# Kernel tuning notes

Measured on AMD Instinct MI355X. Metric: run time of the kernel, lower is better.

The kernel has to match this reference:

```python
import jax, jax.numpy as jnp
import numpy as np

B, H, W, P, DEPTH = 128, 512, 512, 64, 4
EPS = 1e-5


def _std(t):
    # torch.std default: unbiased (ddof=1), over last two dims, keepdim
    m = t.mean(axis=(-2, -1), keepdims=True)
    n = t.shape[-1] * t.shape[-2]
    var = ((t - m) ** 2).sum(axis=(-2, -1), keepdims=True) / (n - 1)
    return jnp.sqrt(var)


def _flat_softmax(t):
    # softmax over all non-batch dims (flatten(1).softmax(1).reshape)
    b = t.shape[0]
    return jax.nn.softmax(t.reshape(b, -1), axis=1).reshape(t.shape)


def setup_inputs() -> dict:
    key = jax.random.key(0)
    ks = jax.random.split(key, 9)
    # xavier-uniform-like scale for [*, fan_in, fan_out] params
    def init(k, shape):
        fan_in, fan_out = shape[-2], shape[-1]
        gain = float(np.sqrt(2.0))  # relu gain
        bound = gain * float(np.sqrt(6.0 / (fan_in + fan_out)))
        return jax.random.uniform(k, shape, jnp.float32, -bound, bound)
    return {
        "x": jax.random.normal(ks[0], (B, H, W), jnp.float32),
        "o_xj": init(ks[1], (DEPTH, W, P)),
        "o_xi": init(ks[2], (DEPTH, H, P)),
        "p_xj": init(ks[3], (DEPTH, H, P)),
        "p_xi": init(ks[4], (DEPTH, W, P)),
        "o_rel_xj": init(ks[5], (DEPTH, W, P)),
        "o_rel_xi": init(ks[6], (DEPTH, H, P)),
        "p_rel_xj": init(ks[7], (DEPTH, P, P)),
        "p_rel_xi": init(ks[8], (DEPTH, P, P)),
    }


def reference(x, o_xj, o_xi, p_xj, p_xi, o_rel_xj, o_rel_xi, p_rel_xj, p_rel_xi):
    # eval-mode forward (dropout inactive)
    b, h, w = x.shape
    p = o_xj.shape[-1]
    depth = o_xj.shape[0]
    scale = (h / p) * (w / p)
    x_mean = x.mean(axis=(-2, -1), keepdims=True) * scale  # [B,1,1]
    x_std = _std(x) * scale                                 # [B,1,1]
    xt = jnp.swapaxes(x, -1, -2)                            # [B,W,H]

    projection = jnp.zeros((b, p, p), jnp.float32)
    for d in range(depth):
        # relevance branches on original orientation
        o_rel_xj_sum = _flat_softmax(x @ o_rel_xj[d]).sum(axis=-2)   # [B,P]
        o_rel_xi_sum = _flat_softmax(xt @ o_rel_xi[d]).sum(axis=-2)  # [B,P]
        # projection branches
        o_t_xj = x @ o_xj[d]                                # [B,H,P]
        o_t_xi = xt @ o_xi[d]                               # [B,W,P]
        p_t_xj = jnp.swapaxes(o_t_xj, -1, -2) @ p_xj[d]     # [B,P,P]
        p_t_xi = jnp.swapaxes(o_t_xi, -1, -2) @ p_xi[d]     # [B,P,P]
        # relevance branches on permuted projection
        p_rel_xj_sum = _flat_softmax(p_t_xj @ p_rel_xj[d]).sum(axis=-2)  # [B,P]
        p_rel_xi_sum = _flat_softmax(p_t_xi @ p_rel_xi[d]).sum(axis=-2)  # [B,P]
        f_j = jnp.sqrt(o_rel_xj_sum / p_rel_xj_sum)         # [B,P]
        f_i = jnp.sqrt(o_rel_xi_sum / p_rel_xi_sum)         # [B,P]
        x_buf = p_t_xj * f_j[..., None] + jnp.swapaxes(p_t_xi * f_i[..., None], -1, -2)
        # renormalize to original (scaled) statistics
        x_buf = (x_buf - x_buf.mean(axis=(-2, -1), keepdims=True)) / (_std(x_buf) + EPS)
        x_buf = x_buf * x_std + x_mean
        projection = projection + x_buf
    return projection
```

## Files before the change

kernel.cpp:

```cpp
#include <hip/hip_runtime.h>
#include <math.h>

typedef __attribute__((ext_vector_type(8))) short short8;
typedef __attribute__((ext_vector_type(4))) short short4v;
typedef __attribute__((ext_vector_type(4))) float f32x4;

#define EPSF 1e-5f

__device__ __forceinline__ short f2bf(float f) {
    union { float f; unsigned u; } v; v.f = f;
    unsigned r = (v.u + 0x7FFFu + ((v.u >> 16) & 1u)) >> 16;
    return (short)r;
}

__device__ __forceinline__ void gload16(const void* g, void* l) {
    __builtin_amdgcn_global_load_lds(
        (const __attribute__((address_space(1))) unsigned int*)g,
        (__attribute__((address_space(3))) unsigned int*)l, 16, 0, 0);
}

__global__ __launch_bounds__(256) void xprep_kernel(const float* __restrict__ x,
                                                    short* __restrict__ xbf,
                                                    short* __restrict__ xtbf,
                                                    double* __restrict__ part) {
    int blk = blockIdx.x;
    int b = blk >> 6, t = blk & 63;
    int tr = (t >> 3) * 64, tc = (t & 7) * 64;
    const float* X = x + (size_t)b * 262144;
    __shared__ short tileR[64][80];
    __shared__ double rs[256], rq[256];
    int tid = threadIdx.x;

    {
        int r = tid >> 2, cseg = (tid & 3) * 16;
        const float* src = X + (size_t)(tr + r) * 512 + tc + cseg;
        double s = 0.0, sq = 0.0;
        short vals[16];
        #pragma unroll
        for (int q = 0; q < 4; q++) {
            float4 f = *(const float4*)(src + q * 4);
            vals[q * 4 + 0] = f2bf(f.x); vals[q * 4 + 1] = f2bf(f.y);
            vals[q * 4 + 2] = f2bf(f.z); vals[q * 4 + 3] = f2bf(f.w);
            s += (double)f.x + (double)f.y + (double)f.z + (double)f.w;
            sq += (double)f.x * f.x + (double)f.y * f.y + (double)f.z * f.z + (double)f.w * f.w;
        }
        *(short8*)&tileR[r][cseg]     = *(short8*)&vals[0];
        *(short8*)&tileR[r][cseg + 8] = *(short8*)&vals[8];
        rs[tid] = s; rq[tid] = sq;
    }
    __syncthreads();
    for (int st = 128; st > 0; st >>= 1) {
        if (tid < st) { rs[tid] += rs[tid + st]; rq[tid] += rq[tid + st]; }
        __syncthreads();
    }
    if (tid == 0) { part[blk * 2] = rs[0]; part[blk * 2 + 1] = rq[0]; }

    int w = tid >> 6, l = tid & 63, li = l & 15, lg = l >> 4;
    #pragma unroll
    for (int q = 0; q < 2; q++) {
        int cc = w * 2 + q;
        int Rl = cc >> 1, ktl = cc & 1;
        short8 v = *(const short8*)&tileR[Rl * 16 + li][ktl * 32 + lg * 8];
        size_t chunk = (size_t)(b * 32 + (tr >> 4) + Rl) * 16 + (tc >> 5) + ktl;
        *(short8*)(xbf + chunk * 512 + l * 8) = v;
    }
    #pragma unroll
    for (int q = 0; q < 2; q++) {
        int cc = w * 2 + q;
        int Rl = cc >> 1, ktl = cc & 1;
        int c_loc = Rl * 16 + li;
        int rbase = ktl * 32 + lg * 8;
        short8 v;
        #pragma unroll
        for (int e = 0; e < 8; e++) v[e] = tileR[rbase + e][c_loc];
        size_t chunk = (size_t)(b * 32 + (tc >> 4) + Rl) * 16 + (tr >> 5) + ktl;
        *(short8*)(xtbf + chunk * 512 + l * 8) = v;
    }
}

__global__ __launch_bounds__(256) void stats_p1(const float* __restrict__ x,
                                                double* __restrict__ part) {
    int blk = blockIdx.x;
    const float4* X = (const float4*)(x + (size_t)blk * 65536);
    double s = 0.0, sq = 0.0;
    for (int i = threadIdx.x; i < 16384; i += 256) {
        float4 v = X[i];
        s += (double)v.x + (double)v.y + (double)v.z + (double)v.w;
        sq += (double)v.x * v.x + (double)v.y * v.y + (double)v.z * v.z + (double)v.w * v.w;
    }
    __shared__ double rs[256], rq[256];
    rs[threadIdx.x] = s; rq[threadIdx.x] = sq;
    __syncthreads();
    for (int st = 128; st > 0; st >>= 1) {
        if (threadIdx.x < st) { rs[threadIdx.x] += rs[threadIdx.x + st]; rq[threadIdx.x] += rq[threadIdx.x + st]; }
        __syncthreads();
    }
    if (threadIdx.x == 0) { part[blk * 2] = rs[0]; part[blk * 2 + 1] = rq[0]; }
}

__global__ void stats_p2(const double* __restrict__ part, float* __restrict__ stats, int ppb) {
    int b = threadIdx.x;
    double s = 0.0, sq = 0.0;
    for (int p = 0; p < ppb; p++) { s += part[(b * ppb + p) * 2]; sq += part[(b * ppb + p) * 2 + 1]; }
    double n = 262144.0;
    double mean = s / n;
    double var = (sq - n * mean * mean) / (n - 1.0);
    stats[b * 2 + 0] = (float)(mean * 64.0);
    stats[b * 2 + 1] = (float)(sqrt(var) * 64.0);
}

__global__ __launch_bounds__(256) void wprep_kernel(
    const float* __restrict__ o_xj, const float* __restrict__ o_xi,
    const float* __restrict__ p_xj, const float* __restrict__ p_xi,
    const float* __restrict__ o_rel_xj, const float* __restrict__ o_rel_xi,
    short* __restrict__ wcat, short* __restrict__ wpt) {
    int idx = blockIdx.x * 256 + threadIdx.x;
    if (idx < 65536) {
        int l = idx & 63; int chunk = idx >> 6;
        int kt = chunk & 15, ns = (chunk >> 4) & 7, sd = chunk >> 7;
        int side = sd >> 2, dd = sd & 3;
        int n = ns * 16 + (l & 15);
        int k = kt * 32 + (l >> 4) * 8;
        const float* src = (n < 64) ? (side ? o_rel_xi : o_rel_xj)
                                    : (side ? o_xi : o_xj);
        src += (size_t)dd * 32768 + (n & 63);
        short8 v;
        #pragma unroll
        for (int e = 0; e < 8; e++) v[e] = f2bf(src[(size_t)(k + e) * 64]);
        *(short8*)(wcat + (size_t)chunk * 512 + l * 8) = v;
    } else {
        int j = idx - 65536;
        int l = j & 63; int chunk = j >> 6;
        int nq = chunk & 3, kk = (chunk >> 2) & 3, mt = (chunk >> 4) & 3, sd = chunk >> 6;
        int side = sd >> 2, dd = sd & 3;
        int q = nq * 16 + (l & 15);
        int r = mt * 128 + kk * 32 + (l >> 4) * 8;
        const float* src = (side ? p_xi : p_xj) + (size_t)dd * 32768 + q;
        short8 v;
        #pragma unroll
        for (int e = 0; e < 8; e++) v[e] = f2bf(src[(size_t)(r + e) * 64]);
        *(short8*)(wpt + (size_t)chunk * 512 + l * 8) = v;
    }
}

__global__ __launch_bounds__(256, 3) void main_mfma_kernel(
    const short* __restrict__ xbf, const short* __restrict__ xtbf,
    const short* __restrict__ wcat, const short* __restrict__ wpt,
    float* __restrict__ relsum, float* __restrict__ pt) {
    int blk = blockIdx.x;
    int xcd = blk & 7, rest = blk >> 3;
    int d = rest & 3, side = (rest >> 2) & 1, bhi = rest >> 3;
    int b = bhi * 8 + xcd;
    const short* Xsw = (side ? xtbf : xbf) + (size_t)b * 262144;
    const short* Wc  = wcat + (size_t)(side * 4 + d) * 65536;
    const short* Wp  = wpt + (size_t)(side * 4 + d) * 32768;

    __shared__ __align__(16) char lds[33792];
    short* Xs  = (short*)lds;
    short* Wsh = (short*)(lds + 8192);
    short* Tos = (short*)lds;
    short* Wps = (short*)(lds + 17408);

    int tid = threadIdx.x;
    int w = tid >> 6, l = tid & 63, li = l & 15, lg = l >> 4;
    int wm = w >> 1, wn = w & 1;

    f32x4 zero4 = {0.f, 0.f, 0.f, 0.f};
    f32x4 ptacc[4];
    #pragma unroll
    for (int i = 0; i < 4; i++) ptacc[i] = zero4;
    float esum[4] = {0.f, 0.f, 0.f, 0.f};

    for (int mt = 0; mt < 4; mt++) {
        f32x4 acc[4][4];
        #pragma unroll
        for (int i = 0; i < 4; i++)
            #pragma unroll
            for (int j = 0; j < 4; j++) acc[i][j] = zero4;

        for (int kt = 0; kt < 16; kt++) {
            __syncthreads();
            #pragma unroll
            for (int ii = 0; ii < 4; ii++) {
                int s = w * 4 + ii;
                if (s < 8)
                    gload16(Xsw + ((size_t)((mt * 8 + s) * 16 + kt)) * 512 + l * 8, Xs + s * 512);
                else
                    gload16(Wc + ((size_t)((s - 8) * 16 + kt)) * 512 + l * 8, Wsh + (s - 8) * 512);
            }
            __syncthreads();
            short8 af[4], bfv[4];
            #pragma unroll
            for (int i = 0; i < 4; i++) af[i] = *(const short8*)(Xs + (wm * 4 + i) * 512 + l * 8);
            #pragma unroll
            for (int j = 0; j < 4; j++) bfv[j] = *(const short8*)(Wsh + (wn * 4 + j) * 512 + l * 8);
            #pragma unroll
            for (int i = 0; i < 4; i++)
                #pragma unroll
                for (int j = 0; j < 4; j++)
                    acc[i][j] = __builtin_amdgcn_mfma_f32_16x16x32_bf16(af[i], bfv[j], acc[i][j], 0, 0, 0);
        }

        #pragma unroll
        for (int ii = 0; ii < 4; ii++) {
            int s = w * 4 + ii;
            gload16(Wp + ((size_t)((mt * 4 + (s >> 2)) * 4 + (s & 3))) * 512 + l * 8, Wps + s * 512);
        }
        __syncthreads();

        if (wn == 0) {
            #pragma unroll
            for (int i = 0; i < 4; i++)
                #pragma unroll
                for (int j = 0; j < 4; j++)
                    esum[j] += __expf(acc[i][j][0]) + __expf(acc[i][j][1]) +
                               __expf(acc[i][j][2]) + __expf(acc[i][j][3]);
        } else {
            #pragma unroll
            for (int i = 0; i < 4; i++)
                #pragma unroll
                for (int j = 0; j < 4; j++) {
                    int p = j * 16 + li;
                    int rb = wm * 64 + i * 16 + lg * 4;
                    short4v tv;
                    tv.x = f2bf(acc[i][j][0]); tv.y = f2bf(acc[i][j][1]);
                    tv.z = f2bf(acc[i][j][2]); tv.w = f2bf(acc[i][j][3]);
                    *(short4v*)(Tos + p * 136 + rb) = tv;
                }
        }
        __syncthreads();

        #pragma unroll
        for (int kk = 0; kk < 4; kk++) {
            short8 a = *(const short8*)(Tos + (w * 16 + li) * 136 + kk * 32 + lg * 8);
            #pragma unroll
            for (int nq = 0; nq < 4; nq++) {
                short8 bb = *(const short8*)(Wps + (kk * 4 + nq) * 512 + l * 8);
                ptacc[nq] = __builtin_amdgcn_mfma_f32_16x16x32_bf16(a, bb, ptacc[nq], 0, 0, 0);
            }
        }
    }

    __syncthreads();
    float* red = (float*)lds;
    if (wn == 0) {
        #pragma unroll
        for (int j = 0; j < 4; j++) red[wm * 256 + l * 4 + j] = esum[j];
    }
    __syncthreads();
    size_t base = (size_t)(b * 2 + side) * 4 + d;
    if (tid < 64) {
        float s = 0.f;
        #pragma unroll
        for (int w2 = 0; w2 < 2; w2++)
            #pragma unroll
            for (int g = 0; g < 4; g++)
                s += red[w2 * 256 + (g * 16 + (tid & 15)) * 4 + (tid >> 4)];
        float tot = s;
        #pragma unroll
        for (int off = 1; off < 64; off <<= 1) tot += __shfl_xor(tot, off, 64);
        relsum[base * 64 + tid] = s / tot;
    }
    float* ptout = pt + base * 4096;
    #pragma unroll
    for (int nq = 0; nq < 4; nq++)
        #pragma unroll
        for (int r = 0; r < 4; r++)
            ptout[(size_t)(w * 16 + lg * 4 + r) * 64 + nq * 16 + li] = ptacc[nq][r];
}

__global__ __launch_bounds__(256) void fused_proj_kernel(
    const float* __restrict__ x,
    const float* __restrict__ o_xj, const float* __restrict__ o_xi,
    const float* __restrict__ p_xj, const float* __restrict__ p_xi,
    const float* __restrict__ o_rel_xj, const float* __restrict__ o_rel_xi,
    float* __restrict__ relsum, float* __restrict__ pt)
{
    int blk = blockIdx.x;
    int b = blk >> 3;
    int side = (blk >> 2) & 1;
    int d = blk & 3;

    const float* Wrel = (side ? o_rel_xi : o_rel_xj) + (size_t)d * (512 * 64);
    const float* Wo   = (side ? o_xi     : o_xj)     + (size_t)d * (512 * 64);
    const float* Wp   = (side ? p_xi     : p_xj)     + (size_t)d * (512 * 64);
    const float* X = x + (size_t)b * (512 * 512);

    __shared__ float Xs[16][68];
    __shared__ float Ws[16][128];
    __shared__ float To[64][68];
    __shared__ float Wps[64][68];
    __shared__ float red[16][64];
    __shared__ float cs[64];
    __shared__ float total_s;

    int tid = threadIdx.x;
    int tx = tid & 15;
    int ty = tid >> 4;

    float paccum[4][4];
    #pragma unroll
    for (int i = 0; i < 4; i++)
        #pragma unroll
        for (int j = 0; j < 4; j++) paccum[i][j] = 0.f;
    float esum[8];
    #pragma unroll
    for (int j = 0; j < 8; j++) esum[j] = 0.f;

    for (int r0 = 0; r0 < 512; r0 += 64) {
        float acc[4][8];
        #pragma unroll
        for (int i = 0; i < 4; i++)
            #pragma unroll
            for (int j = 0; j < 8; j++) acc[i][j] = 0.f;

        for (int k0 = 0; k0 < 512; k0 += 16) {
            if (side == 0) {
                int kk = tid & 15, r = tid >> 4;
                #pragma unroll
                for (int it = 0; it < 4; it++, r += 16)
                    Xs[kk][r] = X[(size_t)(r0 + r) * 512 + (k0 + kk)];
            } else {
                int r = tid & 63, kk = tid >> 6;
                #pragma unroll
                for (int it = 0; it < 4; it++, kk += 4)
                    Xs[kk][r] = X[(size_t)(k0 + kk) * 512 + (r0 + r)];
            }
            {
                int c = tid & 127, kk = tid >> 7;
                const float* Wsrc = (c < 64) ? (Wrel + c) : (Wo + (c - 64));
                #pragma unroll
                for (int it = 0; it < 8; it++, kk += 2)
                    Ws[kk][c] = Wsrc[(size_t)(k0 + kk) * 64];
            }
            __syncthreads();
            #pragma unroll
            for (int kk = 0; kk < 16; kk++) {
                float4 a  = *(const float4*)&Xs[kk][ty * 4];
                float4 b0 = *(const float4*)&Ws[kk][tx * 8];
                float4 b1 = *(const float4*)&Ws[kk][tx * 8 + 4];
                float av[4] = {a.x, a.y, a.z, a.w};
                float bv[8] = {b0.x, b0.y, b0.z, b0.w, b1.x, b1.y, b1.z, b1.w};
                #pragma unroll
                for (int i = 0; i < 4; i++)
                    #pragma unroll
                    for (int j = 0; j < 8; j++)
                        acc[i][j] = fmaf(av[i], bv[j], acc[i][j]);
            }
            __syncthreads();
        }

        if (tx < 8) {
            #pragma unroll
            for (int i = 0; i < 4; i++)
                #pragma unroll
                for (int j = 0; j < 8; j++)
                    esum[j] += expf(acc[i][j]);
        } else {
            #pragma unroll
            for (int i = 0; i < 4; i++) {
                float4 v0 = make_float4(acc[i][0], acc[i][1], acc[i][2], acc[i][3]);
                float4 v1 = make_float4(acc[i][4], acc[i][5], acc[i][6], acc[i][7]);
                *(float4*)&To[ty * 4 + i][(tx - 8) * 8]     = v0;
                *(float4*)&To[ty * 4 + i][(tx - 8) * 8 + 4] = v1;
            }
        }
        {
            int q = tid & 63, r = tid >> 6;
            #pragma unroll
            for (int it = 0; it < 16; it++, r += 4)
                Wps[r][q] = Wp[(size_t)(r0 + r) * 64 + q];
        }
        __syncthreads();
        for (int r = 0; r < 64; r++) {
            float4 aa = *(const float4*)&To[r][ty * 4];
            float4 bb = *(const float4*)&Wps[r][tx * 4];
            float av[4] = {aa.x, aa.y, aa.z, aa.w};
            float bv[4] = {bb.x, bb.y, bb.z, bb.w};
            #pragma unroll
            for (int i = 0; i < 4; i++)
                #pragma unroll
                for (int j = 0; j < 4; j++)
                    paccum[i][j] = fmaf(av[i], bv[j], paccum[i][j]);
        }
        __syncthreads();
    }

    if (tx < 8) {
        #pragma unroll
        for (int j = 0; j < 8; j++) red[ty][tx * 8 + j] = esum[j];
    }
    __syncthreads();
    if (tid < 64) {
        float s = 0.f;
        for (int t = 0; t < 16; t++) s += red[t][tid];
        cs[tid] = s;
    }
    __syncthreads();
    if (tid == 0) {
        float tot = 0.f;
        for (int i = 0; i < 64; i++) tot += cs[i];
        total_s = tot;
    }
    __syncthreads();
    size_t base = (size_t)(b * 2 + side) * 4 + d;
    if (tid < 64) relsum[base * 64 + tid] = cs[tid] / total_s;

    float* ptout = pt + base * 4096;
    #pragma unroll
    for (int i = 0; i < 4; i++)
        #pragma unroll
        for (int j = 0; j < 4; j++)
            ptout[(size_t)(ty * 4 + i) * 64 + tx * 4 + j] = paccum[i][j];
}

__global__ __launch_bounds__(256) void finalize2_kernel(
    const float* __restrict__ relsum, float* __restrict__ pt,
    const float* __restrict__ p_rel_xj, const float* __restrict__ p_rel_xi,
    const float* __restrict__ stats)
{
    int blk = blockIdx.x;
    int b = blk >> 2, d = blk & 3;
    int tid = threadIdx.x, tx = tid & 15, ty = tid >> 4;
    __shared__ float Ptj[64][65], Pti[64][65], Wr[64][65];
    __shared__ float red[16][64];
    __shared__ float fj[64], fi[64];
    __shared__ float rs[256], rq[256];
    __shared__ float bc[1];

    float x_mean = stats[b * 2 + 0];
    float x_std  = stats[b * 2 + 1];

    float* ptj = pt + ((size_t)(b * 2 + 0) * 4 + d) * 4096;
    const float* pti = pt + ((size_t)(b * 2 + 1) * 4 + d) * 4096;
    for (int it = 0; it < 16; it++) {
        int idx = tid + it * 256;
        Ptj[idx >> 6][idx & 63] = ptj[idx];
        Pti[idx >> 6][idx & 63] = pti[idx];
    }
    __syncthreads();

    for (int s = 0; s < 2; s++) {
        const float* prel = (s == 0) ? (p_rel_xj + (size_t)d * 4096)
                                     : (p_rel_xi + (size_t)d * 4096);
        for (int it = 0; it < 16; it++) {
            int idx = tid + it * 256;
            Wr[idx >> 6][idx & 63] = prel[idx];
        }
        __syncthreads();
        float cpart[4] = {0.f, 0.f, 0.f, 0.f};
        for (int i = 0; i < 4; i++) {
            int p = ty * 4 + i;
            float q[4] = {0.f, 0.f, 0.f, 0.f};
            for (int r = 0; r < 64; r++) {
                float a = (s == 0) ? Ptj[p][r] : Pti[p][r];
                #pragma unroll
                for (int j = 0; j < 4; j++)
                    q[j] = fmaf(a, Wr[r][tx * 4 + j], q[j]);
            }
            #pragma unroll
            for (int j = 0; j < 4; j++) cpart[j] += __expf(q[j]);
        }
        #pragma unroll
        for (int j = 0; j < 4; j++) red[ty][tx * 4 + j] = cpart[j];
        __syncthreads();
        float* ftgt = (s == 0) ? fj : fi;
        if (tid < 64) {
            float cssum = 0.f;
            for (int t = 0; t < 16; t++) cssum += red[t][tid];
            ftgt[tid] = cssum;
        }
        __syncthreads();
        if (tid == 0) {
            float tot = 0.f;
            for (int i = 0; i < 64; i++) tot += ftgt[i];
            bc[0] = tot;
        }
        __syncthreads();
        if (tid < 64) {
            float prel_sum = ftgt[tid] / bc[0];
            float orel = relsum[((size_t)(b * 2 + s) * 4 + d) * 64 + tid];
            ftgt[tid] = sqrtf(orel / prel_sum);
        }
        __syncthreads();
    }

    float v[4][4];
    float psum = 0.f, psq = 0.f;
    #pragma unroll
    for (int i = 0; i < 4; i++) {
        int r = ty * 4 + i;
        #pragma unroll
        for (int j = 0; j < 4; j++) {
            int c = tx * 4 + j;
            float val = Ptj[r][c] * fj[r] + Pti[c][r] * fi[c];
            v[i][j] = val; psum += val; psq += val * val;
        }
    }
    rs[tid] = psum; rq[tid] = psq;
    __syncthreads();
    for (int st = 128; st > 0; st >>= 1) {
        if (tid < st) { rs[tid] += rs[tid + st]; rq[tid] += rq[tid + st]; }
        __syncthreads();
    }
    float mean = rs[0] / 4096.f;
    float var = (rq[0] - 4096.f * mean * mean) / 4095.f;
    float inv = 1.0f / (sqrtf(var) + EPSF);
    #pragma unroll
    for (int i = 0; i < 4; i++)
        #pragma unroll
        for (int j = 0; j < 4; j++)
            ptj[(size_t)(ty * 4 + i) * 64 + tx * 4 + j] = (v[i][j] - mean) * inv * x_std + x_mean;
}

__global__ __launch_bounds__(256) void sum_kernel(const float* __restrict__ pt,
                                                  float* __restrict__ out) {
    int b = blockIdx.x, tid = threadIdx.x;
    for (int it = 0; it < 16; it++) {
        int idx = tid + it * 256;
        float s = 0.f;
        #pragma unroll
        for (int d = 0; d < 4; d++)
            s += pt[((size_t)(b * 2) * 4 + d) * 4096 + idx];
        out[(size_t)b * 4096 + idx] = s;
    }
}

extern "C" void kernel_launch(void* const* d_in, const int* in_sizes, int n_in,
                              void* d_out, int out_size, void* d_ws, size_t ws_size,
                              hipStream_t stream) {
    const float* x        = (const float*)d_in[0];
    const float* o_xj     = (const float*)d_in[1];
    const float* o_xi     = (const float*)d_in[2];
    const float* p_xj     = (const float*)d_in[3];
    const float* p_xi     = (const float*)d_in[4];
    const float* o_rel_xj = (const float*)d_in[5];
    const float* o_rel_xi = (const float*)d_in[6];
    const float* p_rel_xj = (const float*)d_in[7];
    const float* p_rel_xi = (const float*)d_in[8];
    float* out = (float*)d_out;

    char* ws = (char*)d_ws;
    float*  stats  = (float*)(ws + 0);
    float*  relsum = (float*)(ws + 1024);
    float*  pt     = (float*)(ws + 263168);
    double* spartF = (double*)(ws + 17040384);
    short*  xbf    = (short*)(ws + 17171456);
    short*  xtbf   = (short*)(ws + 84280320);
    short*  wcat   = (short*)(ws + 151389184);
    short*  wptb   = (short*)(ws + 152437760);
    double* spartS = (double*)(ws + 263168);

    const size_t FAST_NEED = 152962048;
    if (ws_size >= FAST_NEED) {
        xprep_kernel<<<8192, 256, 0, stream>>>(x, xbf, xtbf, spartF);
        wprep_kernel<<<384, 256, 0, stream>>>(o_xj, o_xi, p_xj, p_xi, o_rel_xj, o_rel_xi, wcat, wptb);
        stats_p2<<<1, 128, 0, stream>>>(spartF, stats, 64);
        main_mfma_kernel<<<1024, 256, 0, stream>>>(xbf, xtbf, wcat, wptb, relsum, pt);
    } else {
        stats_p1<<<512, 256, 0, stream>>>(x, spartS);
        stats_p2<<<1, 128, 0, stream>>>(spartS, stats, 4);
        fused_proj_kernel<<<1024, 256, 0, stream>>>(x, o_xj, o_xi, p_xj, p_xi,
                                                    o_rel_xj, o_rel_xi, relsum, pt);
    }
    finalize2_kernel<<<512, 256, 0, stream>>>(relsum, pt, p_rel_xj, p_rel_xi, stats);
    sum_kernel<<<128, 256, 0, stream>>>(pt, out);
}
```

Baseline: 367.9 us.

## Merge prep kernels, fold stats into finalize, accumulate output with atomics

Merges the x and weight preparation kernels into one launch and drops the separate stats reduction by having the finalize kernel reduce the per-batch partial sums with wave shuffles. It also removes the final sum kernel: finalize atomically adds each depth's normalized result into the zeroed output. This cuts launch count and avoids writing and re-reading the per-depth projection buffer. The cost is an extra memset, atomic contention from four depths per batch, and non-deterministic float summation order.

```diff
diff --git a/kernel.cpp b/kernel.cpp
--- a/kernel.cpp
+++ b/kernel.cpp
@@ -19,62 +19,95 @@
         (__attribute__((address_space(3))) unsigned int*)l, 16, 0, 0);
 }
 
-__global__ __launch_bounds__(256) void xprep_kernel(const float* __restrict__ x,
-                                                    short* __restrict__ xbf,
-                                                    short* __restrict__ xtbf,
-                                                    double* __restrict__ part) {
-    int blk = blockIdx.x;
-    int b = blk >> 6, t = blk & 63;
-    int tr = (t >> 3) * 64, tc = (t & 7) * 64;
-    const float* X = x + (size_t)b * 262144;
-    __shared__ short tileR[64][80];
-    __shared__ double rs[256], rq[256];
+__global__ __launch_bounds__(256) void prep_kernel(
+    const float* __restrict__ x,
+    const float* __restrict__ o_xj, const float* __restrict__ o_xi,
+    const float* __restrict__ p_xj, const float* __restrict__ p_xi,
+    const float* __restrict__ o_rel_xj, const float* __restrict__ o_rel_xi,
+    short* __restrict__ xbf, short* __restrict__ xtbf,
+    double* __restrict__ part, short* __restrict__ wcat, short* __restrict__ wpt) {
     int tid = threadIdx.x;
-
-    {
-        int r = tid >> 2, cseg = (tid & 3) * 16;
-        const float* src = X + (size_t)(tr + r) * 512 + tc + cseg;
-        double s = 0.0, sq = 0.0;
-        short vals[16];
-        #pragma unroll
-        for (int q = 0; q < 4; q++) {
-            float4 f = *(const float4*)(src + q * 4);
-            vals[q * 4 + 0] = f2bf(f.x); vals[q * 4 + 1] = f2bf(f.y);
-            vals[q * 4 + 2] = f2bf(f.z); vals[q * 4 + 3] = f2bf(f.w);
-            s += (double)f.x + (double)f.y + (double)f.z + (double)f.w;
-            sq += (double)f.x * f.x + (double)f.y * f.y + (double)f.z * f.z + (double)f.w * f.w;
-        }
-        *(short8*)&tileR[r][cseg]     = *(short8*)&vals[0];
-        *(short8*)&tileR[r][cseg + 8] = *(short8*)&vals[8];
-        rs[tid] = s; rq[tid] = sq;
-    }
-    __syncthreads();
-    for (int st = 128; st > 0; st >>= 1) {
-        if (tid < st) { rs[tid] += rs[tid + st]; rq[tid] += rq[tid + st]; }
-        __syncthreads();
-    }
-    if (tid == 0) { part[blk * 2] = rs[0]; part[blk * 2 + 1] = rq[0]; }
-
-    int w = tid >> 6, l = tid & 63, li = l & 15, lg = l >> 4;
-    #pragma unroll
-    for (int q = 0; q < 2; q++) {
-        int cc = w * 2 + q;
-        int Rl = cc >> 1, ktl = cc & 1;
-        short8 v = *(const short8*)&tileR[Rl * 16 + li][ktl * 32 + lg * 8];
-        size_t chunk = (size_t)(b * 32 + (tr >> 4) + Rl) * 16 + (tc >> 5) + ktl;
-        *(short8*)(xbf + chunk * 512 + l * 8) = v;
-    }
-    #pragma unroll
-    for (int q = 0; q < 2; q++) {
-        int cc = w * 2 + q;
-        int Rl = cc >> 1, ktl = cc & 1;
-        int c_loc = Rl * 16 + li;
-        int rbase = ktl * 32 + lg * 8;
-        short8 v;
-        #pragma unroll
-        for (int e = 0; e < 8; e++) v[e] = tileR[rbase + e][c_loc];
-        size_t chunk = (size_t)(b * 32 + (tc >> 4) + Rl) * 16 + (tr >> 5) + ktl;
-        *(short8*)(xtbf + chunk * 512 + l * 8) = v;
+    if (blockIdx.x < 8192) {
+        int blk = blockIdx.x;
+        int b = blk >> 6, t = blk & 63;
+        int tr = (t >> 3) * 64, tc = (t & 7) * 64;
+        const float* X = x + (size_t)b * 262144;
+        __shared__ short tileR[64][80];
+        __shared__ double rs[256], rq[256];
+
+        {
+            int r = tid >> 2, cseg = (tid & 3) * 16;
+            const float* src = X + (size_t)(tr + r) * 512 + tc + cseg;
+            double s = 0.0, sq = 0.0;
+            short vals[16];
+            #pragma unroll
+            for (int q = 0; q < 4; q++) {
+                float4 f = *(const float4*)(src + q * 4);
+                vals[q * 4 + 0] = f2bf(f.x); vals[q * 4 + 1] = f2bf(f.y);
+                vals[q * 4 + 2] = f2bf(f.z); vals[q * 4 + 3] = f2bf(f.w);
+                s += (double)f.x + (double)f.y + (double)f.z + (double)f.w;
+                sq += (double)f.x * f.x + (double)f.y * f.y + (double)f.z * f.z + (double)f.w * f.w;
+            }
+            *(short8*)&tileR[r][cseg]     = *(short8*)&vals[0];
+            *(short8*)&tileR[r][cseg + 8] = *(short8*)&vals[8];
+            rs[tid] = s; rq[tid] = sq;
+        }
+        __syncthreads();
+        for (int st = 128; st > 0; st >>= 1) {
+            if (tid < st) { rs[tid] += rs[tid + st]; rq[tid] += rq[tid + st]; }
+            __syncthreads();
+        }
+        if (tid == 0) { part[blk * 2] = rs[0]; part[blk * 2 + 1] = rq[0]; }
+
+        int w = tid >> 6, l = tid & 63, li = l & 15, lg = l >> 4;
+        #pragma unroll
+        for (int q = 0; q < 2; q++) {
+            int cc = w * 2 + q;
+            int Rl = cc >> 1, ktl = cc & 1;
+            short8 v = *(const short8*)&tileR[Rl * 16 + li][ktl * 32 + lg * 8];
+            size_t chunk = (size_t)(b * 32 + (tr >> 4) + Rl) * 16 + (tc >> 5) + ktl;
+            *(short8*)(xbf + chunk * 512 + l * 8) = v;
+        }
+        #pragma unroll
+        for (int q = 0; q < 2; q++) {
+            int cc = w * 2 + q;
+            int Rl = cc >> 1, ktl = cc & 1;
+            int c_loc = Rl * 16 + li;
+            int rbase = ktl * 32 + lg * 8;
+            short8 v;
+            #pragma unroll
+            for (int e = 0; e < 8; e++) v[e] = tileR[rbase + e][c_loc];
+            size_t chunk = (size_t)(b * 32 + (tc >> 4) + Rl) * 16 + (tr >> 5) + ktl;
+            *(short8*)(xtbf + chunk * 512 + l * 8) = v;
+        }
+    } else {
+        int idx = (blockIdx.x - 8192) * 256 + tid;
+        if (idx < 65536) {
+            int l = idx & 63; int chunk = idx >> 6;
+            int kt = chunk & 15, ns = (chunk >> 4) & 7, sd = chunk >> 7;
+            int side = sd >> 2, dd = sd & 3;
+            int n = ns * 16 + (l & 15);
+            int k = kt * 32 + (l >> 4) * 8;
+            const float* src = (n < 64) ? (side ? o_rel_xi : o_rel_xj)
+                                        : (side ? o_xi : o_xj);
+            src += (size_t)dd * 32768 + (n & 63);
+            short8 v;
+            #pragma unroll
+            for (int e = 0; e < 8; e++) v[e] = f2bf(src[(size_t)(k + e) * 64]);
+            *(short8*)(wcat + (size_t)chunk * 512 + l * 8) = v;
+        } else {
+            int j = idx - 65536;
+            int l = j & 63; int chunk = j >> 6;
+            int nq = chunk & 3, kk = (chunk >> 2) & 3, mt = (chunk >> 4) & 3, sd = chunk >> 6;
+            int side = sd >> 2, dd = sd & 3;
+            int q = nq * 16 + (l & 15);
+            int r = mt * 128 + kk * 32 + (l >> 4) * 8;
+            const float* src = (side ? p_xi : p_xj) + (size_t)dd * 32768 + q;
+            short8 v;
+            #pragma unroll
+            for (int e = 0; e < 8; e++) v[e] = f2bf(src[(size_t)(r + e) * 64]);
+            *(short8*)(wpt + (size_t)chunk * 512 + l * 8) = v;
+        }
     }
 }
 
@@ -107,40 +140,6 @@
     double var = (sq - n * mean * mean) / (n - 1.0);
     stats[b * 2 + 0] = (float)(mean * 64.0);
     stats[b * 2 + 1] = (float)(sqrt(var) * 64.0);
-}
-
-__global__ __launch_bounds__(256) void wprep_kernel(
-    const float* __restrict__ o_xj, const float* __restrict__ o_xi,
-    const float* __restrict__ p_xj, const float* __restrict__ p_xi,
-    const float* __restrict__ o_rel_xj, const float* __restrict__ o_rel_xi,
-    short* __restrict__ wcat, short* __restrict__ wpt) {
-    int idx = blockIdx.x * 256 + threadIdx.x;
-    if (idx < 65536) {
-        int l = idx & 63; int chunk = idx >> 6;
-        int kt = chunk & 15, ns = (chunk >> 4) & 7, sd = chunk >> 7;
-        int side = sd >> 2, dd = sd & 3;
-        int n = ns * 16 + (l & 15);
-        int k = kt * 32 + (l >> 4) * 8;
-        const float* src = (n < 64) ? (side ? o_rel_xi : o_rel_xj)
-                                    : (side ? o_xi : o_xj);
-        src += (size_t)dd * 32768 + (n & 63);
-        short8 v;
-        #pragma unroll
-        for (int e = 0; e < 8; e++) v[e] = f2bf(src[(size_t)(k + e) * 64]);
-        *(short8*)(wcat + (size_t)chunk * 512 + l * 8) = v;
-    } else {
-        int j = idx - 65536;
-        int l = j & 63; int chunk = j >> 6;
-        int nq = chunk & 3, kk = (chunk >> 2) & 3, mt = (chunk >> 4) & 3, sd = chunk >> 6;
-        int side = sd >> 2, dd = sd & 3;
-        int q = nq * 16 + (l & 15);
-        int r = mt * 128 + kk * 32 + (l >> 4) * 8;
-        const float* src = (side ? p_xi : p_xj) + (size_t)dd * 32768 + q;
-        short8 v;
-        #pragma unroll
-        for (int e = 0; e < 8; e++) v[e] = f2bf(src[(size_t)(r + e) * 64]);
-        *(short8*)(wpt + (size_t)chunk * 512 + l * 8) = v;
-    }
 }
 
 __global__ __launch_bounds__(256, 3) void main_mfma_kernel(
@@ -415,9 +414,10 @@
 }
 
 __global__ __launch_bounds__(256) void finalize2_kernel(
-    const float* __restrict__ relsum, float* __restrict__ pt,
+    const float* __restrict__ relsum, const float* __restrict__ pt,
     const float* __restrict__ p_rel_xj, const float* __restrict__ p_rel_xi,
-    const float* __restrict__ stats)
+    const double* __restrict__ part, const float* __restrict__ stats, int ppb,
+    float* __restrict__ out)
 {
     int blk = blockIdx.x;
     int b = blk >> 2, d = blk & 3;
@@ -427,11 +427,31 @@
     __shared__ float fj[64], fi[64];
     __shared__ float rs[256], rq[256];
     __shared__ float bc[1];
-
-    float x_mean = stats[b * 2 + 0];
-    float x_std  = stats[b * 2 + 1];
-
-    float* ptj = pt + ((size_t)(b * 2 + 0) * 4 + d) * 4096;
+    __shared__ float sstat[2];
+
+    if (ppb > 0) {
+        if (tid < 64) {
+            double s = part[(size_t)(b * 64 + tid) * 2];
+            double sq = part[(size_t)(b * 64 + tid) * 2 + 1];
+            #pragma unroll
+            for (int off = 1; off < 64; off <<= 1) {
+                s += __shfl_xor(s, off, 64);
+                sq += __shfl_xor(sq, off, 64);
+            }
+            if (tid == 0) {
+                double n = 262144.0;
+                double mean = s / n;
+                double var = (sq - n * mean * mean) / (n - 1.0);
+                sstat[0] = (float)(mean * 64.0);
+                sstat[1] = (float)(sqrt(var) * 64.0);
+            }
+        }
+    } else if (tid == 0) {
+        sstat[0] = stats[b * 2 + 0];
+        sstat[1] = stats[b * 2 + 1];
+    }
+
+    const float* ptj = pt + ((size_t)(b * 2 + 0) * 4 + d) * 4096;
     const float* pti = pt + ((size_t)(b * 2 + 1) * 4 + d) * 4096;
     for (int it = 0; it < 16; it++) {
         int idx = tid + it * 256;
@@ -439,6 +459,8 @@
         Pti[idx >> 6][idx & 63] = pti[idx];
     }
     __syncthreads();
+    float x_mean = sstat[0];
+    float x_std  = sstat[1];
 
     for (int s = 0; s < 2; s++) {
         const float* prel = (s == 0) ? (p_rel_xj + (size_t)d * 4096)
@@ -506,24 +528,13 @@
     float mean = rs[0] / 4096.f;
     float var = (rq[0] - 4096.f * mean * mean) / 4095.f;
     float inv = 1.0f / (sqrtf(var) + EPSF);
+    float* ob = out + (size_t)b * 4096;
     #pragma unroll
     for (int i = 0; i < 4; i++)
         #pragma unroll
         for (int j = 0; j < 4; j++)
-            ptj[(size_t)(ty * 4 + i) * 64 + tx * 4 + j] = (v[i][j] - mean) * inv * x_std + x_mean;
-}
-
-__global__ __launch_bounds__(256) void sum_kernel(const float* __restrict__ pt,
-                                                  float* __restrict__ out) {
-    int b = blockIdx.x, tid = threadIdx.x;
-    for (int it = 0; it < 16; it++) {
-        int idx = tid + it * 256;
-        float s = 0.f;
-        #pragma unroll
-        for (int d = 0; d < 4; d++)
-            s += pt[((size_t)(b * 2) * 4 + d) * 4096 + idx];
-        out[(size_t)b * 4096 + idx] = s;
-    }
+            atomicAdd(&ob[(size_t)(ty * 4 + i) * 64 + tx * 4 + j],
+                      (v[i][j] - mean) * inv * x_std + x_mean);
 }
 
 extern "C" void kernel_launch(void* const* d_in, const int* in_sizes, int n_in,
@@ -549,20 +560,30 @@
     short*  xtbf   = (short*)(ws + 84280320);
     short*  wcat   = (short*)(ws + 151389184);
     short*  wptb   = (short*)(ws + 152437760);
-    double* spartS = (double*)(ws + 263168);
+    double* spartS = (double*)(ws + 17040384);
+
+    hipMemsetAsync(d_out, 0, (size_t)out_size * sizeof(float), stream);
 
     const size_t FAST_NEED = 152962048;
     if (ws_size >= FAST_NEED) {
-        xprep_kernel<<<8192, 256, 0, stream>>>(x, xbf, xtbf, spartF);
-        wprep_kernel<<<384, 256, 0, stream>>>(o_xj, o_xi, p_xj, p_xi, o_rel_xj, o_rel_xi, wcat, wptb);
-        stats_p2<<<1, 128, 0, stream>>>(spartF, stats, 64);
+        prep_kernel<<<8576, 256, 0, stream>>>(x, o_xj, o_xi, p_xj, p_xi,
+                                              o_rel_xj, o_rel_xi,
+                                              xbf, xtbf, spartF, wcat, wptb);
         main_mfma_kernel<<<1024, 256, 0, stream>>>(xbf, xtbf, wcat, wptb, relsum, pt);
+        finalize2_kernel<<<512, 256, 0, stream>>>(relsum, pt, p_rel_xj, p_rel_xi,
+                                                  spartF, stats, 64, out);
     } else {
-        stats_p1<<<512, 256, 0, stream>>>(x, spartS);
-        stats_p2<<<1, 128, 0, stream>>>(spartS, stats, 4);
+        if (ws_size >= 17171456) {
+            stats_p1<<<512, 256, 0, stream>>>(x, spartS);
+            stats_p2<<<1, 128, 0, stream>>>(spartS, stats, 4);
+        } else {
+            double* sp = (double*)(ws + 263168);
+            stats_p1<<<512, 256, 0, stream>>>(x, sp);
+            stats_p2<<<1, 128, 0, stream>>>(sp, stats, 4);
+        }
         fused_proj_kernel<<<1024, 256, 0, stream>>>(x, o_xj, o_xi, p_xj, p_xi,
                                                     o_rel_xj, o_rel_xi, relsum, pt);
-    }
-    finalize2_kernel<<<512, 256, 0, stream>>>(relsum, pt, p_rel_xj, p_rel_xi, stats);
-    sum_kernel<<<128, 256, 0, stream>>>(pt, out);
-}
+        finalize2_kernel<<<512, 256, 0, stream>>>(relsum, pt, p_rel_xj, p_rel_xi,
+                                                  (const double*)nullptr, stats, 0, out);
+    }
+}
```

Measured after the change: 378.3 us. 1.03x slower.
